# Kernel tuning notes

Hardware: AMD Instinct MI355X
Metric: run time of the kernel (lower is better)

Reference implementation:

```python
import jax, jax.numpy as jnp
import numpy as np

N = 100000
E = 1600000
D_IN = 128
D_H = 128


def setup_inputs() -> dict:
    key = jax.random.key(0)
    ks = jax.random.split(key, 6)
    x = jax.random.normal(ks[0], (N, D_IN), dtype=jnp.float32)
    edge_index = jax.random.randint(ks[1], (2, E), 0, N, dtype=jnp.int64)
    s1 = 1.0 / np.sqrt(D_IN)
    s2 = 1.0 / np.sqrt(D_H)
    W1l = jax.random.normal(ks[2], (D_IN, D_H), dtype=jnp.float32) * s1
    W1r = jax.random.normal(ks[3], (D_IN, D_H), dtype=jnp.float32) * s1
    W2l = jax.random.normal(ks[4], (D_H, D_H), dtype=jnp.float32) * s2
    W2r = jax.random.normal(ks[5], (D_H, D_H), dtype=jnp.float32) * s2
    b1 = jnp.zeros((D_H,), dtype=jnp.float32)
    b2 = jnp.zeros((D_H,), dtype=jnp.float32)
    return {"x": x, "edge_index": edge_index, "W1l": W1l, "b1": b1,
            "W1r": W1r, "W2l": W2l, "b2": b2, "W2r": W2r}


def _sage_conv(x, src, dst, Wl, b, Wr):
    # mean-aggregate neighbor features: messages flow src -> dst
    agg = jax.ops.segment_sum(x[src], dst, num_segments=N)  # [N, d]
    deg = jax.ops.segment_sum(jnp.ones((src.shape[0],), x.dtype), dst,
                              num_segments=N)
    mean = agg / jnp.maximum(deg, 1.0)[:, None]
    # PyG SAGEConv: lin_l(aggr) + lin_r(x); bias lives in lin_l
    return mean @ Wl + b + x @ Wr


def reference(x, edge_index, W1l, b1, W1r, W2l, b2, W2r):
    src, dst = edge_index[0], edge_index[1]
    h = jax.nn.relu(_sage_conv(x, src, dst, W1l, b1, W1r))
    return _sage_conv(h, src, dst, W2l, b2, W2r)
```

## Files before the change

### kernel.cpp

```cpp
#include <hip/hip_runtime.h>


typedef __attribute__((ext_vector_type(8))) short short8;
typedef __attribute__((ext_vector_type(4))) float floatx4;
typedef __attribute__((ext_vector_type(4))) unsigned short ushort4v;

#define BSH1 9
#define CHUNK 8192

__device__ inline unsigned short f2b(float f) {
    unsigned u = __builtin_bit_cast(unsigned, f);
    return (unsigned short)((u + 0x7FFFu + ((u >> 16) & 1u)) >> 16);
}
__device__ inline float blo(unsigned v) { return __builtin_bit_cast(float, v << 16); }
__device__ inline float bhi(unsigned v) { return __builtin_bit_cast(float, v & 0xffff0000u); }

__global__ void detect_kernel(const int* __restrict__ e32, int nelem, int* flag) {
    __shared__ int bad;
    if (threadIdx.x == 0) bad = 0;
    __syncthreads();
    int half = nelem >> 1;
    int viol = 0;
    for (int i = threadIdx.x; i < 4096; i += blockDim.x) {
        long long k = ((long long)i * half) / 4096;
        if (e32[2 * k + 1] != 0) viol++;
    }
    if (viol) atomicAdd(&bad, viol);
    __syncthreads();
    if (threadIdx.x == 0) flag[0] = (bad == 0) ? 1 : 0;
}

__device__ inline void decode_edge(const int* e32, bool is64, int E, int i, int& s, int& d) {
    if (is64) { s = e32[2 * (long long)i]; d = e32[2 * ((long long)E + i)]; }
    else      { s = e32[i];                d = e32[E + i]; }
}

__global__ __launch_bounds__(256) void coarse_count_kernel(const int* __restrict__ e32,
                                                           const int* __restrict__ flag,
                                                           int* __restrict__ bcnt,
                                                           int E, int nb1) {
    extern __shared__ int lh[];
    for (int i = threadIdx.x; i < nb1; i += blockDim.x) lh[i] = 0;
    __syncthreads();
    bool is64 = flag[0] != 0;
    int stride = gridDim.x * blockDim.x;
    for (int i = blockIdx.x * blockDim.x + threadIdx.x; i < E; i += stride) {
        int d = is64 ? e32[2 * ((long long)E + i)] : e32[E + i];
        atomicAdd(&lh[d >> BSH1], 1);
    }
    __syncthreads();
    for (int i = threadIdx.x; i < nb1; i += blockDim.x) {
        int c = lh[i];
        if (c) atomicAdd(&bcnt[i], c);
    }
}

__global__ __launch_bounds__(1024) void scan_kernel(const int* __restrict__ deg,
                                                    int* __restrict__ off,
                                                    int* __restrict__ cursor, int N) {
    __shared__ int wsum[16];
    __shared__ int s_carry;
    int t = threadIdx.x;
    int lane = t & 63, w = t >> 6;
    if (t == 0) s_carry = 0;
    __syncthreads();
    for (int base = 0; base < N; base += 1024) {
        int i = base + t;
        int v = (i < N) ? deg[i] : 0;
        int sc = v;
        #pragma unroll
        for (int o = 1; o < 64; o <<= 1) {
            int u = __shfl_up(sc, o, 64);
            if (lane >= o) sc += u;
        }
        if (lane == 63) wsum[w] = sc;
        __syncthreads();
        int woff = 0;
        for (int j = 0; j < w; ++j) woff += wsum[j];
        int c = s_carry;
        int excl = c + woff + (sc - v);
        if (i < N) { off[i] = excl; cursor[i] = excl; }
        __syncthreads();
        if (t == 1023) s_carry = c + woff + sc;
        __syncthreads();
    }
    if (t == 0) off[N] = s_carry;
}

__global__ __launch_bounds__(256) void coarse_scatter_kernel(const int* __restrict__ e32,
                                                             const int* __restrict__ flag,
                                                             int* __restrict__ bcur,
                                                             int2* __restrict__ pairs,
                                                             int E, int nb1) {
    extern __shared__ int lh[];
    int t = threadIdx.x;
    bool is64 = flag[0] != 0;
    int nchunks = (E + CHUNK - 1) / CHUNK;
    for (int ch = blockIdx.x; ch < nchunks; ch += gridDim.x) {
        int e0 = ch * CHUNK;
        int e1 = min(e0 + CHUNK, E);
        for (int i = t; i < nb1; i += 256) lh[i] = 0;
        __syncthreads();
        for (int i = e0 + t; i < e1; i += 256) {
            int d = is64 ? e32[2 * ((long long)E + i)] : e32[E + i];
            atomicAdd(&lh[d >> BSH1], 1);
        }
        __syncthreads();
        for (int i = t; i < nb1; i += 256) {
            int c = lh[i];
            lh[nb1 + i] = c ? atomicAdd(&bcur[i], c) : 0;
            lh[i] = 0;
        }
        __syncthreads();
        for (int i = e0 + t; i < e1; i += 256) {
            int s, d; decode_edge(e32, is64, E, i, s, d);
            int k = d >> BSH1;
            int r = atomicAdd(&lh[k], 1);
            pairs[lh[nb1 + k] + r] = make_int2(s, d);
        }
        __syncthreads();
    }
}

__global__ __launch_bounds__(256) void fine_csr_kernel(const int2* __restrict__ pairs,
                                                       const int* __restrict__ boff,
                                                       int* __restrict__ off,
                                                       int* __restrict__ csr,
                                                       int N, int nb1, int E) {
    __shared__ int ldeg[512], loff[512];
    __shared__ int wsum[4];
    int b = blockIdx.x;
    if (b >= nb1) return;
    int t = threadIdx.x;
    int p0 = boff[b], p1 = boff[b + 1];
    int base = b << BSH1;
    ldeg[2 * t] = 0; ldeg[2 * t + 1] = 0;
    __syncthreads();
    for (int i = p0 + t; i < p1; i += 256) atomicAdd(&ldeg[pairs[i].y & 511], 1);
    __syncthreads();
    {
        int lane = t & 63, w = t >> 6;
        int v0 = ldeg[2 * t], v1 = ldeg[2 * t + 1];
        int v = v0 + v1, sc = v;
        #pragma unroll
        for (int o = 1; o < 64; o <<= 1) {
            int u = __shfl_up(sc, o, 64);
            if (lane >= o) sc += u;
        }
        if (lane == 63) wsum[w] = sc;
        __syncthreads();
        int cross = 0;
        for (int j = 0; j < w; ++j) cross += wsum[j];
        int ex = cross + sc - v;
        loff[2 * t] = ex;
        loff[2 * t + 1] = ex + v0;
        int d0 = base + 2 * t, d1 = d0 + 1;
        if (d0 < N) off[d0] = p0 + ex;
        if (d1 < N) off[d1] = p0 + ex + v0;
    }
    __syncthreads();
    ldeg[2 * t] = 0; ldeg[2 * t + 1] = 0;
    __syncthreads();
    for (int i = p0 + t; i < p1; i += 256) {
        int2 e = pairs[i];
        int dl = e.y & 511;
        int r = atomicAdd(&ldeg[dl], 1);
        csr[p0 + loff[dl] + r] = e.x;
    }
    if (b == 0 && t == 0) off[N] = E;
}

__global__ void cvt_kernel(const float* __restrict__ in, unsigned short* __restrict__ out, int n4) {
    int stride = gridDim.x * blockDim.x;
    for (int i = blockIdx.x * blockDim.x + threadIdx.x; i < n4; i += stride) {
        float4 v = ((const float4*)in)[i];
        ushort4v o;
        o[0] = f2b(v.x); o[1] = f2b(v.y); o[2] = f2b(v.z); o[3] = f2b(v.w);
        ((ushort4v*)out)[i] = o;
    }
}

template<int BF16IN>
__global__ __launch_bounds__(256) void spmm_mean_kernel(const void* __restrict__ Xv,
                                                        const int* __restrict__ off,
                                                        const int* __restrict__ csr,
                                                        unsigned* __restrict__ outb, int N) {
    int wid = blockIdx.x * 4 + (threadIdx.x >> 6);
    int lane = threadIdx.x & 63;
    if (wid >= N) return;
    int b0 = off[wid], b1 = off[wid + 1];
    float ax = 0.f, ay = 0.f;
    int i = b0;
    if (BF16IN) {
        const unsigned* X = (const unsigned*)Xv;
        for (; i + 3 < b1; i += 4) {
            int s0 = csr[i], s1 = csr[i + 1], s2 = csr[i + 2], s3 = csr[i + 3];
            unsigned v0 = X[(long long)s0 * 64 + lane];
            unsigned v1 = X[(long long)s1 * 64 + lane];
            unsigned v2 = X[(long long)s2 * 64 + lane];
            unsigned v3 = X[(long long)s3 * 64 + lane];
            ax += blo(v0) + blo(v1) + blo(v2) + blo(v3);
            ay += bhi(v0) + bhi(v1) + bhi(v2) + bhi(v3);
        }
        for (; i < b1; ++i) {
            unsigned v = X[(long long)csr[i] * 64 + lane];
            ax += blo(v); ay += bhi(v);
        }
    } else {
        const float2* X = (const float2*)Xv;
        for (; i + 3 < b1; i += 4) {
            int s0 = csr[i], s1 = csr[i + 1], s2 = csr[i + 2], s3 = csr[i + 3];
            float2 v0 = X[(long long)s0 * 64 + lane];
            float2 v1 = X[(long long)s1 * 64 + lane];
            float2 v2 = X[(long long)s2 * 64 + lane];
            float2 v3 = X[(long long)s3 * 64 + lane];
            ax += v0.x + v1.x + v2.x + v3.x;
            ay += v0.y + v1.y + v2.y + v3.y;
        }
        for (; i < b1; ++i) {
            float2 v = X[(long long)csr[i] * 64 + lane];
            ax += v.x; ay += v.y;
        }
    }
    int dgr = b1 - b0;
    float inv = (dgr > 0) ? 1.0f / (float)dgr : 0.0f;
    unsigned pack = (unsigned)f2b(ax * inv) | ((unsigned)f2b(ay * inv) << 16);
    outb[(long long)wid * 64 + lane] = pack;
}

#define WT_SZ   (128 * 264)
#define APANEL  (64 * 136)
#define ABUF    (2 * APANEL)
#define GEMM_LDS ((WT_SZ + 2 * ABUF) * 2)

template<int XF32, int OUTMODE>
__global__ __launch_bounds__(256, 1) void gemm_mfma_kernel(
    const unsigned short* __restrict__ Am, const void* __restrict__ Ax,
    const float* __restrict__ Wl, const float* __restrict__ Wr,
    const float* __restrict__ bias, void* __restrict__ Out,
    int N, int ntiles)
{
    extern __shared__ unsigned short lds[];
    unsigned short* Wt = lds;
    int t = threadIdx.x;
    int lane = t & 63, wv = t >> 6;
    int lm = lane & 15, q = lane >> 4;
    int c0 = wv * 32;

    for (int it = 0; it < 64; ++it) {
        int n = t & 127;
        int kp = it * 2 + (t >> 7);
        int k = 2 * kp;
        const float* Wsrc = (k < 128) ? (Wl + k * 128) : (Wr + (k - 128) * 128);
        unsigned pack = (unsigned)f2b(Wsrc[n]) | ((unsigned)f2b(Wsrc[128 + n]) << 16);
        *(unsigned*)(Wt + n * 264 + k) = pack;
    }

    float bias0 = bias[c0 + lm];
    float bias1 = bias[c0 + 16 + lm];

    short8 pm[4], px[4];
    auto prefetch = [&](int tl) {
        long long row0 = (long long)tl * 64;
        #pragma unroll
        for (int j = 0; j < 4; ++j) {
            int cid = j * 256 + t;
            int row = cid >> 4, cp = cid & 15;
            long long gr = row0 + row;
            bool ok = gr < (long long)N;
            pm[j] = ok ? *(const short8*)(Am + gr * 128 + cp * 8) : (short8)0;
            if (XF32) {
                short8 s = (short8)0;
                if (ok) {
                    const float* xp = (const float*)Ax + gr * 128 + cp * 8;
                    floatx4 u0 = *(const floatx4*)xp;
                    floatx4 u1 = *(const floatx4*)(xp + 4);
                    s[0] = (short)f2b(u0[0]); s[1] = (short)f2b(u0[1]);
                    s[2] = (short)f2b(u0[2]); s[3] = (short)f2b(u0[3]);
                    s[4] = (short)f2b(u1[0]); s[5] = (short)f2b(u1[1]);
                    s[6] = (short)f2b(u1[2]); s[7] = (short)f2b(u1[3]);
                }
                px[j] = s;
            } else {
                px[j] = ok ? *(const short8*)((const unsigned short*)Ax + gr * 128 + cp * 8)
                           : (short8)0;
            }
        }
    };

    int tile = blockIdx.x;
    if (tile < ntiles) prefetch(tile);
    int buf = 0;
    for (; tile < ntiles; tile += gridDim.x) {
        unsigned short* A = lds + WT_SZ + buf * ABUF;
        __syncthreads();
        #pragma unroll
        for (int j = 0; j < 4; ++j) {
            int cid = j * 256 + t;
            int row = cid >> 4, cp = cid & 15;
            *(short8*)(A + row * 136 + cp * 8) = pm[j];
            *(short8*)(A + APANEL + row * 136 + cp * 8) = px[j];
        }
        __syncthreads();
        int nt = tile + gridDim.x;
        if (nt < ntiles) prefetch(nt);

        floatx4 acc[4][2];
        #pragma unroll
        for (int rf = 0; rf < 4; ++rf) {
            acc[rf][0] = (floatx4)bias0;
            acc[rf][1] = (floatx4)bias1;
        }
        #pragma unroll
        for (int ks = 0; ks < 8; ++ks) {
            const unsigned short* P = A + (ks >= 4 ? APANEL : 0);
            int k0 = (ks & 3) * 32 + q * 8;
            short8 b0 = *(const short8*)(Wt + (c0 + lm) * 264 + ks * 32 + q * 8);
            short8 b1 = *(const short8*)(Wt + (c0 + 16 + lm) * 264 + ks * 32 + q * 8);
            #pragma unroll
            for (int rf = 0; rf < 4; ++rf) {
                short8 a = *(const short8*)(P + (rf * 16 + lm) * 136 + k0);
                acc[rf][0] = __builtin_amdgcn_mfma_f32_16x16x32_bf16(a, b0, acc[rf][0], 0, 0, 0);
                acc[rf][1] = __builtin_amdgcn_mfma_f32_16x16x32_bf16(a, b1, acc[rf][1], 0, 0, 0);
            }
        }

        long long r0 = (long long)tile * 64;
        #pragma unroll
        for (int rf = 0; rf < 4; ++rf) {
            #pragma unroll
            for (int cf = 0; cf < 2; ++cf) {
                int col = c0 + cf * 16 + lm;
                #pragma unroll
                for (int rg = 0; rg < 4; ++rg) {
                    long long rr = r0 + rf * 16 + q * 4 + rg;
                    if (rr < (long long)N) {
                        float v = acc[rf][cf][rg];
                        if (OUTMODE != 2) v = fmaxf(v, 0.f);
                        if (OUTMODE == 1)
                            ((unsigned short*)Out)[rr * 128 + col] = f2b(v);
                        else
                            ((float*)Out)[rr * 128 + col] = v;
                    }
                }
            }
        }
        buf ^= 1;
    }
}

extern "C" void kernel_launch(void* const* d_in, const int* in_sizes, int n_in,
                              void* d_out, int out_size, void* d_ws, size_t ws_size,
                              hipStream_t stream) {
    const float* x   = (const float*)d_in[0];
    const int*   eix = (const int*)d_in[1];
    const float* W1l = (const float*)d_in[2];
    const float* b1  = (const float*)d_in[3];
    const float* W1r = (const float*)d_in[4];
    const float* W2l = (const float*)d_in[5];
    const float* b2  = (const float*)d_in[6];
    const float* W2r = (const float*)d_in[7];
    float* out = (float*)d_out;

    int N = in_sizes[0] / 128;
    int E = in_sizes[1] / 2;
    if (N <= 0 || E <= 0) return;
    int nb1 = (N + (1 << BSH1) - 1) >> BSH1;

    char* ws = (char*)d_ws;
    size_t o = 0;
    auto alloc = [&](size_t bytes) -> void* {
        o = (o + 255) & ~(size_t)255;
        void* p = ws + o;
        o += bytes;
        return p;
    };
    int*            flag   = (int*)alloc(4);
    int*            bcnt   = (int*)alloc((size_t)nb1 * 4);
    int*            boff   = (int*)alloc(((size_t)nb1 + 1) * 4);
    int*            bcur   = (int*)alloc((size_t)nb1 * 4);
    int*            off    = (int*)alloc(((size_t)N + 1) * 4);
    int*            csr    = (int*)alloc((size_t)E * 4);
    unsigned short* xb     = (unsigned short*)alloc((size_t)N * 128 * 2);
    unsigned short* meanb  = (unsigned short*)alloc((size_t)N * 128 * 2);
    unsigned short* hb     = (unsigned short*)alloc((size_t)N * 128 * 2);
    bool full = (o <= ws_size);
    int2* pairs = (int2*)meanb;

    (void)hipFuncSetAttribute((const void*)gemm_mfma_kernel<0, 0>,
                              hipFuncAttributeMaxDynamicSharedMemorySize, GEMM_LDS);
    (void)hipFuncSetAttribute((const void*)gemm_mfma_kernel<0, 1>,
                              hipFuncAttributeMaxDynamicSharedMemorySize, GEMM_LDS);
    (void)hipFuncSetAttribute((const void*)gemm_mfma_kernel<0, 2>,
                              hipFuncAttributeMaxDynamicSharedMemorySize, GEMM_LDS);
    (void)hipFuncSetAttribute((const void*)gemm_mfma_kernel<1, 2>,
                              hipFuncAttributeMaxDynamicSharedMemorySize, GEMM_LDS);

    hipMemsetAsync(bcnt, 0, (size_t)nb1 * 4, stream);

    detect_kernel<<<1, 256, 0, stream>>>(eix, in_sizes[1], flag);
    size_t cnt_lds = (size_t)nb1 * 4;
    coarse_count_kernel<<<256, 256, cnt_lds, stream>>>(eix, flag, bcnt, E, nb1);
    scan_kernel<<<1, 1024, 0, stream>>>(bcnt, boff, bcur, nb1);
    int nchunks = (E + CHUNK - 1) / CHUNK;
    int sgrid = nchunks < 2048 ? nchunks : 2048;
    coarse_scatter_kernel<<<sgrid, 256, 2 * cnt_lds, stream>>>(eix, flag, bcur, pairs, E, nb1);
    fine_csr_kernel<<<nb1, 256, 0, stream>>>(pairs, boff, off, csr, N, nb1, E);

    cvt_kernel<<<2048, 256, 0, stream>>>(x, xb, N * 32);

    int spmm_grid = (N + 3) / 4;
    int ntiles = (N + 63) / 64;
    int ggrid = ntiles < 256 ? ntiles : 256;

    spmm_mean_kernel<1><<<spmm_grid, 256, 0, stream>>>(xb, off, csr, (unsigned*)meanb, N);
    if (full) {
        gemm_mfma_kernel<0, 1><<<ggrid, 256, GEMM_LDS, stream>>>(
            meanb, xb, W1l, W1r, b1, hb, N, ntiles);
        spmm_mean_kernel<1><<<spmm_grid, 256, 0, stream>>>(hb, off, csr, (unsigned*)meanb, N);
        gemm_mfma_kernel<0, 2><<<ggrid, 256, GEMM_LDS, stream>>>(
            meanb, hb, W2l, W2r, b2, out, N, ntiles);
    } else {
        gemm_mfma_kernel<0, 0><<<ggrid, 256, GEMM_LDS, stream>>>(
            meanb, xb, W1l, W1r, b1, out, N, ntiles);
        spmm_mean_kernel<0><<<spmm_grid, 256, 0, stream>>>(out, off, csr, (unsigned*)meanb, N);
        gemm_mfma_kernel<1, 2><<<ggrid, 256, GEMM_LDS, stream>>>(
            meanb, out, W2l, W2r, b2, out, N, ntiles);
    }
}
```

Measured before the change: 287.4 us.

## Pack edge pairs to 32 bits, unroll SpMM by 8, widen GEMM to 512 threads

Edge (src, local-dst) pairs are packed into one 32-bit word (23-bit src, 9-bit dst offset), which halves the traffic of the coarse-scatter and fine-CSR passes. The bf16 SpMM gather loop is unrolled to 8 neighbors so more loads are in flight per wave. The MFMA GEMM now runs 8 waves of 512 threads, each owning 16 output columns instead of 32, which splits the work across more waves at the cost of more A-fragment LDS reads per MFMA. The packing assumes node ids fit in 23 bits.

```diff
diff --git a/kernel.cpp b/kernel.cpp
--- a/kernel.cpp
+++ b/kernel.cpp
@@ -90,7 +90,7 @@
 __global__ __launch_bounds__(256) void coarse_scatter_kernel(const int* __restrict__ e32,
                                                              const int* __restrict__ flag,
                                                              int* __restrict__ bcur,
-                                                             int2* __restrict__ pairs,
+                                                             unsigned* __restrict__ pairs,
                                                              int E, int nb1) {
     extern __shared__ int lh[];
     int t = threadIdx.x;
@@ -116,13 +116,13 @@
             int s, d; decode_edge(e32, is64, E, i, s, d);
             int k = d >> BSH1;
             int r = atomicAdd(&lh[k], 1);
-            pairs[lh[nb1 + k] + r] = make_int2(s, d);
-        }
-        __syncthreads();
-    }
-}
-
-__global__ __launch_bounds__(256) void fine_csr_kernel(const int2* __restrict__ pairs,
+            pairs[lh[nb1 + k] + r] = (unsigned)s | ((unsigned)(d & ((1 << BSH1) - 1)) << 23);
+        }
+        __syncthreads();
+    }
+}
+
+__global__ __launch_bounds__(256) void fine_csr_kernel(const unsigned* __restrict__ pairs,
                                                        const int* __restrict__ boff,
                                                        int* __restrict__ off,
                                                        int* __restrict__ csr,
@@ -136,7 +136,7 @@
     int base = b << BSH1;
     ldeg[2 * t] = 0; ldeg[2 * t + 1] = 0;
     __syncthreads();
-    for (int i = p0 + t; i < p1; i += 256) atomicAdd(&ldeg[pairs[i].y & 511], 1);
+    for (int i = p0 + t; i < p1; i += 256) atomicAdd(&ldeg[pairs[i] >> 23], 1);
     __syncthreads();
     {
         int lane = t & 63, w = t >> 6;
@@ -162,10 +162,10 @@
     ldeg[2 * t] = 0; ldeg[2 * t + 1] = 0;
     __syncthreads();
     for (int i = p0 + t; i < p1; i += 256) {
-        int2 e = pairs[i];
-        int dl = e.y & 511;
+        unsigned e = pairs[i];
+        int dl = e >> 23;
         int r = atomicAdd(&ldeg[dl], 1);
-        csr[p0 + loff[dl] + r] = e.x;
+        csr[p0 + loff[dl] + r] = (int)(e & 0x7FFFFFu);
     }
     if (b == 0 && t == 0) off[N] = E;
 }
@@ -193,6 +193,22 @@
     int i = b0;
     if (BF16IN) {
         const unsigned* X = (const unsigned*)Xv;
+        for (; i + 7 < b1; i += 8) {
+            int s0 = csr[i],     s1 = csr[i + 1], s2 = csr[i + 2], s3 = csr[i + 3];
+            int s4 = csr[i + 4], s5 = csr[i + 5], s6 = csr[i + 6], s7 = csr[i + 7];
+            unsigned v0 = X[(long long)s0 * 64 + lane];
+            unsigned v1 = X[(long long)s1 * 64 + lane];
+            unsigned v2 = X[(long long)s2 * 64 + lane];
+            unsigned v3 = X[(long long)s3 * 64 + lane];
+            unsigned v4 = X[(long long)s4 * 64 + lane];
+            unsigned v5 = X[(long long)s5 * 64 + lane];
+            unsigned v6 = X[(long long)s6 * 64 + lane];
+            unsigned v7 = X[(long long)s7 * 64 + lane];
+            ax += (blo(v0) + blo(v1)) + (blo(v2) + blo(v3)) +
+                  ((blo(v4) + blo(v5)) + (blo(v6) + blo(v7)));
+            ay += (bhi(v0) + bhi(v1)) + (bhi(v2) + bhi(v3)) +
+                  ((bhi(v4) + bhi(v5)) + (bhi(v6) + bhi(v7)));
+        }
         for (; i + 3 < b1; i += 4) {
             int s0 = csr[i], s1 = csr[i + 1], s2 = csr[i + 2], s3 = csr[i + 3];
             unsigned v0 = X[(long long)s0 * 64 + lane];
@@ -234,7 +250,7 @@
 #define GEMM_LDS ((WT_SZ + 2 * ABUF) * 2)
 
 template<int XF32, int OUTMODE>
-__global__ __launch_bounds__(256, 1) void gemm_mfma_kernel(
+__global__ __launch_bounds__(512, 1) void gemm_mfma_kernel(
     const unsigned short* __restrict__ Am, const void* __restrict__ Ax,
     const float* __restrict__ Wl, const float* __restrict__ Wr,
     const float* __restrict__ bias, void* __restrict__ Out,
@@ -245,11 +261,11 @@
     int t = threadIdx.x;
     int lane = t & 63, wv = t >> 6;
     int lm = lane & 15, q = lane >> 4;
-    int c0 = wv * 32;
-
-    for (int it = 0; it < 64; ++it) {
+    int c0 = wv * 16;
+
+    for (int it = 0; it < 32; ++it) {
         int n = t & 127;
-        int kp = it * 2 + (t >> 7);
+        int kp = it * 4 + (t >> 7);
         int k = 2 * kp;
         const float* Wsrc = (k < 128) ? (Wl + k * 128) : (Wr + (k - 128) * 128);
         unsigned pack = (unsigned)f2b(Wsrc[n]) | ((unsigned)f2b(Wsrc[128 + n]) << 16);
@@ -257,14 +273,13 @@
     }
 
     float bias0 = bias[c0 + lm];
-    float bias1 = bias[c0 + 16 + lm];
-
-    short8 pm[4], px[4];
+
+    short8 pm[2], px[2];
     auto prefetch = [&](int tl) {
         long long row0 = (long long)tl * 64;
         #pragma unroll
-        for (int j = 0; j < 4; ++j) {
-            int cid = j * 256 + t;
+        for (int j = 0; j < 2; ++j) {
+            int cid = j * 512 + t;
             int row = cid >> 4, cp = cid & 15;
             long long gr = row0 + row;
             bool ok = gr < (long long)N;
@@ -295,8 +310,8 @@
         unsigned short* A = lds + WT_SZ + buf * ABUF;
         __syncthreads();
         #pragma unroll
-        for (int j = 0; j < 4; ++j) {
-            int cid = j * 256 + t;
+        for (int j = 0; j < 2; ++j) {
+            int cid = j * 512 + t;
             int row = cid >> 4, cp = cid & 15;
             *(short8*)(A + row * 136 + cp * 8) = pm[j];
             *(short8*)(A + APANEL + row * 136 + cp * 8) = px[j];
@@ -305,43 +320,35 @@
         int nt = tile + gridDim.x;
         if (nt < ntiles) prefetch(nt);
 
-        floatx4 acc[4][2];
-        #pragma unroll
-        for (int rf = 0; rf < 4; ++rf) {
-            acc[rf][0] = (floatx4)bias0;
-            acc[rf][1] = (floatx4)bias1;
-        }
+        floatx4 acc[4];
+        #pragma unroll
+        for (int rf = 0; rf < 4; ++rf) acc[rf] = (floatx4)bias0;
         #pragma unroll
         for (int ks = 0; ks < 8; ++ks) {
             const unsigned short* P = A + (ks >= 4 ? APANEL : 0);
             int k0 = (ks & 3) * 32 + q * 8;
             short8 b0 = *(const short8*)(Wt + (c0 + lm) * 264 + ks * 32 + q * 8);
-            short8 b1 = *(const short8*)(Wt + (c0 + 16 + lm) * 264 + ks * 32 + q * 8);
             #pragma unroll
             for (int rf = 0; rf < 4; ++rf) {
                 short8 a = *(const short8*)(P + (rf * 16 + lm) * 136 + k0);
-                acc[rf][0] = __builtin_amdgcn_mfma_f32_16x16x32_bf16(a, b0, acc[rf][0], 0, 0, 0);
-                acc[rf][1] = __builtin_amdgcn_mfma_f32_16x16x32_bf16(a, b1, acc[rf][1], 0, 0, 0);
+                acc[rf] = __builtin_amdgcn_mfma_f32_16x16x32_bf16(a, b0, acc[rf], 0, 0, 0);
             }
         }
 
         long long r0 = (long long)tile * 64;
+        int col = c0 + lm;
         #pragma unroll
         for (int rf = 0; rf < 4; ++rf) {
             #pragma unroll
-            for (int cf = 0; cf < 2; ++cf) {
-                int col = c0 + cf * 16 + lm;
-                #pragma unroll
-                for (int rg = 0; rg < 4; ++rg) {
-                    long long rr = r0 + rf * 16 + q * 4 + rg;
-                    if (rr < (long long)N) {
-                        float v = acc[rf][cf][rg];
-                        if (OUTMODE != 2) v = fmaxf(v, 0.f);
-                        if (OUTMODE == 1)
-                            ((unsigned short*)Out)[rr * 128 + col] = f2b(v);
-                        else
-                            ((float*)Out)[rr * 128 + col] = v;
-                    }
+            for (int rg = 0; rg < 4; ++rg) {
+                long long rr = r0 + rf * 16 + q * 4 + rg;
+                if (rr < (long long)N) {
+                    float v = acc[rf][rg];
+                    if (OUTMODE != 2) v = fmaxf(v, 0.f);
+                    if (OUTMODE == 1)
+                        ((unsigned short*)Out)[rr * 128 + col] = f2b(v);
+                    else
+                        ((float*)Out)[rr * 128 + col] = v;
                 }
             }
         }
@@ -385,7 +392,7 @@
     unsigned short* meanb  = (unsigned short*)alloc((size_t)N * 128 * 2);
     unsigned short* hb     = (unsigned short*)alloc((size_t)N * 128 * 2);
     bool full = (o <= ws_size);
-    int2* pairs = (int2*)meanb;
+    unsigned* pairs = (unsigned*)meanb;
 
     (void)hipFuncSetAttribute((const void*)gemm_mfma_kernel<0, 0>,
                               hipFuncAttributeMaxDynamicSharedMemorySize, GEMM_LDS);
@@ -415,16 +422,16 @@
 
     spmm_mean_kernel<1><<<spmm_grid, 256, 0, stream>>>(xb, off, csr, (unsigned*)meanb, N);
     if (full) {
-        gemm_mfma_kernel<0, 1><<<ggrid, 256, GEMM_LDS, stream>>>(
+        gemm_mfma_kernel<0, 1><<<ggrid, 512, GEMM_LDS, stream>>>(
             meanb, xb, W1l, W1r, b1, hb, N, ntiles);
         spmm_mean_kernel<1><<<spmm_grid, 256, 0, stream>>>(hb, off, csr, (unsigned*)meanb, N);
-        gemm_mfma_kernel<0, 2><<<ggrid, 256, GEMM_LDS, stream>>>(
+        gemm_mfma_kernel<0, 2><<<ggrid, 512, GEMM_LDS, stream>>>(
             meanb, hb, W2l, W2r, b2, out, N, ntiles);
     } else {
-        gemm_mfma_kernel<0, 0><<<ggrid, 256, GEMM_LDS, stream>>>(
+        gemm_mfma_kernel<0, 0><<<ggrid, 512, GEMM_LDS, stream>>>(
             meanb, xb, W1l, W1r, b1, out, N, ntiles);
         spmm_mean_kernel<0><<<spmm_grid, 256, 0, stream>>>(out, off, csr, (unsigned*)meanb, N);
-        gemm_mfma_kernel<1, 2><<<ggrid, 256, GEMM_LDS, stream>>>(
+        gemm_mfma_kernel<1, 2><<<ggrid, 512, GEMM_LDS, stream>>>(
             meanb, out, W2l, W2r, b2, out, N, ntiles);
     }
 }
```

Result: faster. 258.9 us (-9.9%).
